# Optimization experiments

Hardware: AMD Instinct MI355X
Metric: run time of the kernel (lower is better)

The kernel has to match this reference:

```python
import jax, jax.numpy as jnp
import numpy as np

B, D, H, W, C = 8, 4, 56, 56, 128
HEADS = 4
WD, WH, WW = 2, 7, 7
SD, SH, SW = 1, 3, 3
N = WD * WH * WW            # tokens per window = 98
NW = (D // WD) * (H // WH) * (W // WW)  # windows per sample = 128
SCALE = (C // HEADS) ** -0.5
EPS = 1e-5


def _rel_pos_index():
    coords = np.stack(np.meshgrid(np.arange(WD), np.arange(WH), np.arange(WW), indexing='ij'))
    coords = coords.reshape(3, -1)                    # (3, N)
    rel = (coords[:, :, None] - coords[:, None, :]).transpose(1, 2, 0)  # (N, N, 3)
    rel[:, :, 0] += WD - 1
    rel[:, :, 1] += WH - 1
    rel[:, :, 2] += WW - 1
    rel[:, :, 0] *= (2 * WH - 1) * (2 * WW - 1)
    rel[:, :, 1] *= (2 * WW - 1)
    return rel.sum(-1)                                # (N, N) int

REL_IDX = jnp.asarray(_rel_pos_index())


def _np_window_partition(x, wd, wh, ww):
    b, d, h, w, c = x.shape
    x = x.reshape(b, d // wd, wd, h // wh, wh, w // ww, ww, c)
    return x.transpose(0, 1, 3, 5, 2, 4, 6, 7).reshape(-1, wd * wh * ww, c)


def _attn_mask():
    img = np.zeros((1, D, H, W, 1), np.float32)
    cnt = 0
    for ds in (slice(None, -WD), slice(-WD, -SD), slice(-SD, None)):
        for hs in (slice(None, -WH), slice(-WH, -SH), slice(-SH, None)):
            for ws in (slice(None, -WW), slice(-WW, -SW), slice(-SW, None)):
                img[:, ds, hs, ws, :] = cnt
                cnt += 1
    mw = _np_window_partition(img, WD, WH, WW)[..., 0]         # (nW, N)
    m = mw[:, None, :] - mw[:, :, None]                        # (nW, N, N)
    return jnp.asarray(np.where(m != 0, -100.0, 0.0).astype(np.float32))

ATTN_MASK = _attn_mask()  # (nW, N, N)


def window_partition(x):
    b = x.shape[0]
    x = x.reshape(b, D // WD, WD, H // WH, WH, W // WW, WW, C)
    return x.transpose(0, 1, 3, 5, 2, 4, 6, 7).reshape(-1, N, C)


def window_reverse(wins, b):
    x = wins.reshape(b, D // WD, H // WH, W // WW, WD, WH, WW, C)
    return x.transpose(0, 1, 4, 2, 5, 3, 6, 7).reshape(b, D, H, W, C)


def layernorm(x, g, b):
    mu = jnp.mean(x, axis=-1, keepdims=True)
    var = jnp.mean(jnp.square(x - mu), axis=-1, keepdims=True)
    return (x - mu) / jnp.sqrt(var + EPS) * g + b


def swin_block(x, norm1_g, norm1_b, qkv_w, qkv_b, rpb_table, proj_w, proj_b,
               norm2_g, norm2_b, fc1_w, fc1_b, fc2_w, fc2_b):
    shortcut = x
    h1 = layernorm(x, norm1_g, norm1_b)
    # cyclic shift (pad amounts are 0 for these dims)
    shifted = jnp.roll(h1, (-SD, -SH, -SW), axis=(1, 2, 3))
    xw = window_partition(shifted)                    # (B*nW, N, C)
    Bn = xw.shape[0]
    qkv = (xw @ qkv_w + qkv_b).reshape(Bn, N, 3, HEADS, C // HEADS)
    qkv = qkv.transpose(2, 0, 3, 1, 4)                # (3, Bn, h, N, c)
    q, k, v = qkv[0], qkv[1], qkv[2]
    attn = jnp.einsum('bhnc,bhmc->bhnm', q * SCALE, k)
    bias = rpb_table[REL_IDX].transpose(2, 0, 1)      # (h, N, N)
    attn = attn + bias[None]
    attn = attn.reshape(B, NW, HEADS, N, N) + ATTN_MASK[None, :, None]
    attn = jax.nn.softmax(attn.reshape(Bn, HEADS, N, N), axis=-1)
    out = jnp.einsum('bhnm,bhmc->bhnc', attn, v)
    out = out.transpose(0, 2, 1, 3).reshape(Bn, N, C)
    out = out @ proj_w + proj_b
    xr = window_reverse(out, B)
    xr = jnp.roll(xr, (SD, SH, SW), axis=(1, 2, 3))
    x1 = shortcut + xr
    h2 = layernorm(x1, norm2_g, norm2_b)
    mlp = jax.nn.gelu(h2 @ fc1_w + fc1_b, approximate=False) @ fc2_w + fc2_b
    return x1 + mlp


def setup_inputs() -> dict:
    key = jax.random.key(0)
    ks = jax.random.split(key, 6)
    s = 0.02
    return {
        'x': jax.random.normal(ks[0], (B, D, H, W, C), jnp.float32),
        'norm1_g': jnp.ones((C,), jnp.float32),
        'norm1_b': jnp.zeros((C,), jnp.float32),
        'qkv_w': jax.random.normal(ks[1], (C, 3 * C), jnp.float32) * s,
        'qkv_b': jnp.zeros((3 * C,), jnp.float32),
        'rpb_table': jax.random.normal(ks[2], ((2 * WD - 1) * (2 * WH - 1) * (2 * WW - 1), HEADS), jnp.float32) * s,
        'proj_w': jax.random.normal(ks[3], (C, C), jnp.float32) * s,
        'proj_b': jnp.zeros((C,), jnp.float32),
        'norm2_g': jnp.ones((C,), jnp.float32),
        'norm2_b': jnp.zeros((C,), jnp.float32),
        'fc1_w': jax.random.normal(ks[4], (C, 4 * C), jnp.float32) * s,
        'fc1_b': jnp.zeros((4 * C,), jnp.float32),
        'fc2_w': jax.random.normal(ks[5], (4 * C, C), jnp.float32) * s,
        'fc2_b': jnp.zeros((C,), jnp.float32),
    }


def reference(x, norm1_g, norm1_b, qkv_w, qkv_b, rpb_table, proj_w, proj_b,
              norm2_g, norm2_b, fc1_w, fc1_b, fc2_w, fc2_b):
    return swin_block(x, norm1_g, norm1_b, qkv_w, qkv_b, rpb_table, proj_w, proj_b,
                      norm2_g, norm2_b, fc1_w, fc1_b, fc2_w, fc2_b)
```

## Files before the change

### kernel.cpp

```cpp
#include <hip/hip_runtime.h>
#include <hip/hip_bf16.h>
#include <cstdint>
#include <cstddef>

using bf16 = __hip_bfloat16;
typedef __bf16 bf16x8 __attribute__((ext_vector_type(8)));
typedef float f32x4 __attribute__((ext_vector_type(4)));

#define DEV static __device__ __forceinline__

DEV bf16 f2b(float x) { return __float2bfloat16(x); }
DEV f32x4 mfma16(bf16x8 a, bf16x8 b, f32x4 c) {
    return __builtin_amdgcn_mfma_f32_16x16x32_bf16(a, b, c, 0, 0, 0);
}
DEV float gelu_f(float x) {
    float u2 = x * x;
    float u = x * (0.7978845608028654f + 0.0356774081363001f * u2);
    float s = 1.f / (1.f + __expf(-2.f * u));
    return x * s;
}
DEV void gload16(const bf16* g, bf16* l) {
    __builtin_amdgcn_global_load_lds(
        (const __attribute__((address_space(1))) unsigned int*)g,
        (__attribute__((address_space(3))) unsigned int*)l, 16, 0, 0);
}
DEV void stage16k(const bf16* __restrict__ g, bf16* l, int tid) {
    int w = tid >> 6, lane = tid & 63;
    #pragma unroll
    for (int j = 0; j < 4; ++j) {
        int blk = j * 4 + w;
        gload16(g + blk * 512 + lane * 8, l + blk * 512);
    }
}

constexpr int NTOK = 98;
constexpr int BNWIN = 1024;
constexpr int MTOT = BNWIN * NTOK;
constexpr float SCALE = 0.17677669529663687f;
constexpr float EPS = 1e-5f;

__global__ __launch_bounds__(256) void k_prep(const float* __restrict__ qkv_w,
        const float* __restrict__ proj_w, const float* __restrict__ fc1_w,
        const float* __restrict__ fc2_w, const float* __restrict__ rpb,
        bf16* __restrict__ QW, bf16* __restrict__ PW,
        bf16* __restrict__ W1, bf16* __restrict__ W2, float* __restrict__ BT) {
    int tid = blockIdx.x * 256 + threadIdx.x;
    int stride = gridDim.x * 256;
    for (int i = tid; i < 384 * 128; i += stride) {
        int n = i >> 7, k = i & 127;
        QW[i] = f2b(qkv_w[k * 384 + n]);
    }
    for (int i = tid; i < 128 * 128; i += stride) {
        int n = i >> 7, k = i & 127;
        PW[i] = f2b(proj_w[k * 128 + n]);
    }
    for (int i = tid; i < 512 * 128; i += stride) {
        int t = i >> 13, r = (i >> 7) & 63, kswz = i & 127;
        int k = kswz ^ ((r & 7) << 3);
        W1[i] = f2b(fc1_w[(size_t)k * 512 + t * 64 + r]);
    }
    for (int i = tid; i < 512 * 128; i += stride) {
        int t = i >> 13, c = (i >> 6) & 127, kswz = i & 63;
        int kk = kswz ^ ((c & 7) << 3);
        W2[i] = f2b(fc2_w[(size_t)(t * 64 + kk) * 128 + c]);
    }
    for (int i = tid; i < 4 * 98 * 98; i += stride) {
        int h = i / 9604, r = i - h * 9604;
        int ii = r / 98, jj = r - ii * 98;
        int di = ii >= 49, ri = ii - di * 49, hi = ri / 7, wi = ri - hi * 7;
        int dj = jj >= 49, rj = jj - dj * 49, hj = rj / 7, wj = rj - hj * 7;
        int bidx = (di - dj + 1) * 169 + (hi - hj + 6) * 13 + (wi - wj + 6);
        BT[i] = rpb[bidx * 4 + h];
    }
}

__global__ __launch_bounds__(256) void k_ln1(const float* __restrict__ x,
        const float* __restrict__ g, const float* __restrict__ be,
        bf16* __restrict__ xw) {
    int wave = threadIdx.x >> 6, lane = threadIdx.x & 63;
    int r = blockIdx.x * 4 + wave;
    int bn = r / 98, n = r - bn * 98;
    int b = bn >> 7, wr = bn & 127;
    int dB = wr >> 6, hB = (wr >> 3) & 7, wB = wr & 7;
    int dd = (n >= 49), rem = n - dd * 49;
    int hh = rem / 7, ww = rem - hh * 7;
    int dp = dB * 2 + dd, hp = hB * 7 + hh, wp = wB * 7 + ww;
    int ds = (dp + 1) & 3;
    int hs = hp + 3; if (hs >= 56) hs -= 56;
    int wsv = wp + 3; if (wsv >= 56) wsv -= 56;
    size_t src = ((size_t)((b * 4 + ds) * 56 + hs) * 56 + wsv) * 128;

    float2 v = *(const float2*)&x[src + lane * 2];
    float v0 = v.x, v1 = v.y;
    float s = v0 + v1, sq = v0 * v0 + v1 * v1;
    #pragma unroll
    for (int m = 1; m < 64; m <<= 1) { s += __shfl_xor(s, m); sq += __shfl_xor(sq, m); }
    float mean = s * (1.f / 128.f);
    float var = sq * (1.f / 128.f) - mean * mean;
    float rstd = rsqrtf(var + EPS);
    float g0 = g[lane * 2], g1 = g[lane * 2 + 1];
    float e0 = be[lane * 2], e1 = be[lane * 2 + 1];
    union { uint32_t u32; bf16 h[2]; } o;
    o.h[0] = f2b((v0 - mean) * rstd * g0 + e0);
    o.h[1] = f2b((v1 - mean) * rstd * g1 + e1);
    *(uint32_t*)&xw[(size_t)r * 128 + lane * 2] = o.u32;
}

__global__ __launch_bounds__(256) void k_qkv(const bf16* __restrict__ A,
        const bf16* __restrict__ QW, const float* __restrict__ bias,
        bf16* __restrict__ out) {
    __shared__ __align__(16) bf16 As[64 * 136];
    __shared__ __align__(16) bf16 Bt[64 * 136];
    int tid = threadIdx.x;
    int row0 = blockIdx.x * 64;
    int col0 = blockIdx.y * 64;
    #pragma unroll
    for (int p = 0; p < 4; ++p) {
        int vi = tid + p * 256;
        int row = vi >> 4, cg = vi & 15;
        *(uint4*)&As[row * 136 + cg * 8] =
            *(const uint4*)&A[(size_t)(row0 + row) * 128 + cg * 8];
    }
    #pragma unroll
    for (int p = 0; p < 4; ++p) {
        int vi = tid + p * 256;
        int row = vi >> 4, cg = vi & 15;
        *(uint4*)&Bt[row * 136 + cg * 8] =
            *(const uint4*)&QW[(size_t)(col0 + row) * 128 + cg * 8];
    }
    __syncthreads();
    int wave = tid >> 6, lane = tid & 63;
    int wr = (wave >> 1) * 32, wc = (wave & 1) * 32;
    int lrow = lane & 15, kg8 = (lane >> 4) * 8, g4 = (lane >> 4) * 4;
    f32x4 acc[2][2] = {};
    #pragma unroll
    for (int ksi = 0; ksi < 4; ++ksi) {
        bf16x8 a[2], bb[2];
        #pragma unroll
        for (int t = 0; t < 2; ++t)
            a[t] = *(const bf16x8*)&As[(wr + t * 16 + lrow) * 136 + ksi * 32 + kg8];
        #pragma unroll
        for (int u2 = 0; u2 < 2; ++u2)
            bb[u2] = *(const bf16x8*)&Bt[(wc + u2 * 16 + lrow) * 136 + ksi * 32 + kg8];
        #pragma unroll
        for (int t = 0; t < 2; ++t)
            #pragma unroll
            for (int u2 = 0; u2 < 2; ++u2)
                acc[t][u2] = mfma16(a[t], bb[u2], acc[t][u2]);
    }
    #pragma unroll
    for (int t = 0; t < 2; ++t)
        #pragma unroll
        for (int u2 = 0; u2 < 2; ++u2) {
            int gcol = col0 + wc + u2 * 16 + lrow;
            float bv = bias[gcol];
            #pragma unroll
            for (int r2 = 0; r2 < 4; ++r2) {
                int grow = row0 + wr + t * 16 + g4 + r2;
                out[(size_t)grow * 384 + gcol] = f2b(acc[t][u2][r2] + bv);
            }
        }
}

__global__ __launch_bounds__(256) void k_attn(const bf16* __restrict__ qkv,
        const float* __restrict__ BT, bf16* __restrict__ aout) {
    __shared__ __align__(16) bf16 qs[112 * 40];
    __shared__ __align__(16) bf16 ksm[112 * 40];
    __shared__ __align__(16) bf16 vt[32 * 136];
    __shared__ __align__(16) bf16 ps[112 * 136];
    __shared__ signed char trg[112];

    int tid = threadIdx.x;
    int bn = blockIdx.x, h = blockIdx.y;
    int wrw = bn & 127;
    int dB = wrw >> 6, hB = (wrw >> 3) & 7, wB = wrw & 7;

    {
        uint32_t* z1 = (uint32_t*)qs;
        uint32_t* z2 = (uint32_t*)ksm;
        for (int i = tid; i < 2240; i += 256) { z1[i] = 0u; z2[i] = 0u; }
        uint32_t* z3 = (uint32_t*)vt;
        for (int i = tid; i < 2176; i += 256) z3[i] = 0u;
        uint32_t* z4 = (uint32_t*)ps;
        for (int i = tid; i < 7616; i += 256) z4[i] = 0u;
    }
    if (tid < 112) {
        int n = tid < 98 ? tid : 97;
        int dd = n >= 49, rem = n - dd * 49;
        int hh = rem / 7, ww2 = rem - hh * 7;
        int dp = dB * 2 + dd, hp = hB * 7 + hh, wp = wB * 7 + ww2;
        int rd = dp < 2 ? 0 : (dp == 2 ? 1 : 2);
        int rh = hp < 49 ? 0 : (hp < 53 ? 1 : 2);
        int rw = wp < 49 ? 0 : (wp < 53 ? 1 : 2);
        trg[tid] = (signed char)(rd * 9 + rh * 3 + rw);
    }
    __syncthreads();
    const size_t base = (size_t)bn * 98 * 384 + h * 32;
    for (int ch = tid; ch < 1176; ch += 256) {
        int mat = ch / 392;
        int rem = ch - mat * 392;
        int row = rem >> 2, cg = rem & 3;
        uint4 v = *(const uint4*)&qkv[base + (size_t)row * 384 + mat * 128 + cg * 8];
        if (mat == 0)      *(uint4*)&qs[row * 40 + cg * 8] = v;
        else if (mat == 1) *(uint4*)&ksm[row * 40 + cg * 8] = v;
        else {
            const bf16* pv = (const bf16*)&v;
            #pragma unroll
            for (int j = 0; j < 8; ++j) vt[(cg * 8 + j) * 136 + row] = pv[j];
        }
    }
    __syncthreads();

    int wave = tid >> 6, lane = tid & 63;
    int lrow = lane & 15, kg8 = (lane >> 4) * 8, g4 = (lane >> 4) * 4;

    for (int rt = wave; rt < 7; rt += 4) {
        f32x4 sacc[7];
        bf16x8 qa = *(const bf16x8*)&qs[(rt * 16 + lrow) * 40 + kg8];
        #pragma unroll
        for (int ct = 0; ct < 7; ++ct) {
            bf16x8 kb = *(const bf16x8*)&ksm[(ct * 16 + lrow) * 40 + kg8];
            f32x4 z = {};
            sacc[ct] = mfma16(qa, kb, z);
        }
        #pragma unroll
        for (int r2 = 0; r2 < 4; ++r2) {
            int grow = rt * 16 + g4 + r2;
            int mi = grow < 98 ? grow : 97;
            int mrg = trg[mi];
            const float* btrow = &BT[((size_t)h * 98 + mi) * 98];
            float val[7];
            float mx = -1e30f;
            #pragma unroll
            for (int ct = 0; ct < 7; ++ct) {
                int jc = ct * 16 + lrow;
                int jj = jc < 98 ? jc : 97;
                float bias = btrow[jj];
                float mv = (mrg != (int)trg[jj]) ? -100.f : 0.f;
                float v = sacc[ct][r2] * SCALE + bias + mv;
                if (jc >= 98) v = -1e30f;
                val[ct] = v;
                mx = fmaxf(mx, v);
            }
            #pragma unroll
            for (int m = 1; m < 16; m <<= 1) mx = fmaxf(mx, __shfl_xor(mx, m));
            float sum = 0.f;
            #pragma unroll
            for (int ct = 0; ct < 7; ++ct) { val[ct] = __expf(val[ct] - mx); sum += val[ct]; }
            #pragma unroll
            for (int m = 1; m < 16; m <<= 1) sum += __shfl_xor(sum, m);
            float inv = 1.f / sum;
            #pragma unroll
            for (int ct = 0; ct < 7; ++ct)
                ps[grow * 136 + ct * 16 + lrow] = f2b(val[ct] * inv);
        }
        #pragma unroll
        for (int ct = 0; ct < 2; ++ct) {
            f32x4 oacc = {};
            #pragma unroll
            for (int ksi = 0; ksi < 4; ++ksi) {
                bf16x8 pa = *(const bf16x8*)&ps[(rt * 16 + lrow) * 136 + ksi * 32 + kg8];
                bf16x8 vb = *(const bf16x8*)&vt[(ct * 16 + lrow) * 136 + ksi * 32 + kg8];
                oacc = mfma16(pa, vb, oacc);
            }
            #pragma unroll
            for (int r2 = 0; r2 < 4; ++r2) {
                int grow = rt * 16 + g4 + r2;
                if (grow < 98)
                    aout[((size_t)bn * 98 + grow) * 128 + h * 32 + ct * 16 + lrow] =
                        f2b(oacc[r2]);
            }
        }
    }
}

__global__ __launch_bounds__(256) void k_proj(const bf16* __restrict__ A,
        const bf16* __restrict__ PW, const float* __restrict__ pb,
        const float* __restrict__ x, const float* __restrict__ g2,
        const float* __restrict__ be2,
        float* __restrict__ x1, bf16* __restrict__ h2) {
    __shared__ __align__(16) bf16 As[64 * 136];
    __shared__ __align__(16) bf16 Bt[128 * 136];
    int tid = threadIdx.x;
    int row0 = blockIdx.x * 64;
    #pragma unroll
    for (int p = 0; p < 4; ++p) {
        int vi = tid + p * 256;
        int row = vi >> 4, cg = vi & 15;
        *(uint4*)&As[row * 136 + cg * 8] =
            *(const uint4*)&A[(size_t)(row0 + row) * 128 + cg * 8];
    }
    #pragma unroll
    for (int p = 0; p < 8; ++p) {
        int vi = tid + p * 256;
        int row = vi >> 4, cg = vi & 15;
        *(uint4*)&Bt[row * 136 + cg * 8] =
            *(const uint4*)&PW[(size_t)row * 128 + cg * 8];
    }
    __syncthreads();
    int wave = tid >> 6, lane = tid & 63;
    int lrow = lane & 15, kg8 = (lane >> 4) * 8, g4 = (lane >> 4) * 4;
    f32x4 acc[8] = {};
    #pragma unroll
    for (int ksi = 0; ksi < 4; ++ksi) {
        bf16x8 a = *(const bf16x8*)&As[(wave * 16 + lrow) * 136 + ksi * 32 + kg8];
        #pragma unroll
        for (int ct = 0; ct < 8; ++ct) {
            bf16x8 bb = *(const bf16x8*)&Bt[(ct * 16 + lrow) * 136 + ksi * 32 + kg8];
            acc[ct] = mfma16(a, bb, acc[ct]);
        }
    }
    #pragma unroll
    for (int r2 = 0; r2 < 4; ++r2) {
        int rwin = row0 + wave * 16 + g4 + r2;
        int bn = rwin / 98, n = rwin - bn * 98;
        int b = bn >> 7, wr2 = bn & 127;
        int dB = wr2 >> 6, hB = (wr2 >> 3) & 7, wB = wr2 & 7;
        int dd = n >= 49, rem = n - dd * 49;
        int hh = rem / 7, ww2 = rem - hh * 7;
        int dp = dB * 2 + dd, hp = hB * 7 + hh, wp = wB * 7 + ww2;
        int d2 = (dp + 1) & 3;
        int hv = hp + 3; if (hv >= 56) hv -= 56;
        int wv = wp + 3; if (wv >= 56) wv -= 56;
        size_t dst = ((size_t)(b * 4 + d2) * 56 + hv) * 56 + wv;
        float vals[8], s = 0.f, sq = 0.f;
        #pragma unroll
        for (int ct = 0; ct < 8; ++ct) {
            int col = ct * 16 + lrow;
            float v = acc[ct][r2] + pb[col] + x[dst * 128 + col];
            vals[ct] = v; s += v; sq += v * v;
        }
        #pragma unroll
        for (int m = 1; m < 16; m <<= 1) { s += __shfl_xor(s, m); sq += __shfl_xor(sq, m); }
        float mean = s * (1.f / 128.f);
        float var = sq * (1.f / 128.f) - mean * mean;
        float rstd = rsqrtf(var + EPS);
        #pragma unroll
        for (int ct = 0; ct < 8; ++ct) {
            int col = ct * 16 + lrow;
            x1[dst * 128 + col] = vals[ct];
            h2[dst * 128 + col] = f2b((vals[ct] - mean) * rstd * g2[col] + be2[col]);
        }
    }
}

__global__ __launch_bounds__(256, 2) void k_mlp(const bf16* __restrict__ h2,
        const bf16* __restrict__ W1s, const float* __restrict__ b1,
        const bf16* __restrict__ W2s, const float* __restrict__ b2v,
        const float* __restrict__ x1, float* __restrict__ out) {
    __shared__ __align__(16) bf16 W1b[2][8192];
    __shared__ __align__(16) bf16 W2b[2][8192];
    __shared__ __align__(16) bf16 Ts[64 * 72];
    int tid = threadIdx.x;
    int row0 = blockIdx.x * 64;
    int wave = tid >> 6, lane = tid & 63;
    int lrow = lane & 15, kg8 = (lane >> 4) * 8, g4 = (lane >> 4) * 4;
    int swz = (lrow & 7) << 3;

    stage16k(W1s, W1b[0], tid);
    stage16k(W2s, W2b[0], tid);

    bf16x8 a1[4];
    const bf16* arow = &h2[(size_t)(row0 + wave * 16 + lrow) * 128];
    #pragma unroll
    for (int ksi = 0; ksi < 4; ++ksi)
        a1[ksi] = *(const bf16x8*)&arow[ksi * 32 + kg8];

    __syncthreads();

    f32x4 oacc[8] = {};
    int n = 0;
    for (int hc = 0; hc < 8; ++hc) {
        if (hc < 7) {
            stage16k(W1s + (hc + 1) * 8192, W1b[n ^ 1], tid);
            stage16k(W2s + (hc + 1) * 8192, W2b[n ^ 1], tid);
        }
        f32x4 tacc[4] = {};
        #pragma unroll
        for (int ksi = 0; ksi < 4; ++ksi) {
            int k0 = ksi * 32 + kg8;
            #pragma unroll
            for (int ct = 0; ct < 4; ++ct) {
                bf16x8 bb = *(const bf16x8*)&W1b[n][(ct * 16 + lrow) * 128 + (k0 ^ swz)];
                tacc[ct] = mfma16(a1[ksi], bb, tacc[ct]);
            }
        }
        #pragma unroll
        for (int ct = 0; ct < 4; ++ct) {
            int hcol = hc * 64 + ct * 16 + lrow;
            float bb = b1[hcol];
            #pragma unroll
            for (int r2 = 0; r2 < 4; ++r2) {
                float t = gelu_f(tacc[ct][r2] + bb);
                Ts[(wave * 16 + g4 + r2) * 72 + ct * 16 + lrow] = f2b(t);
            }
        }
        #pragma unroll
        for (int ksi = 0; ksi < 2; ++ksi) {
            int k0 = ksi * 32 + kg8;
            bf16x8 a = *(const bf16x8*)&Ts[(wave * 16 + lrow) * 72 + k0];
            #pragma unroll
            for (int ct = 0; ct < 8; ++ct) {
                bf16x8 bb = *(const bf16x8*)&W2b[n][(ct * 16 + lrow) * 64 + (k0 ^ swz)];
                oacc[ct] = mfma16(a, bb, oacc[ct]);
            }
        }
        __syncthreads();
        n ^= 1;
    }
    #pragma unroll
    for (int ct = 0; ct < 8; ++ct) {
        int col = ct * 16 + lrow;
        float bb = b2v[col];
        #pragma unroll
        for (int r2 = 0; r2 < 4; ++r2) {
            size_t grow = (size_t)row0 + wave * 16 + g4 + r2;
            out[grow * 128 + col] = oacc[ct][r2] + bb + x1[grow * 128 + col];
        }
    }
}

extern "C" void kernel_launch(void* const* d_in, const int* in_sizes, int n_in,
                              void* d_out, int out_size, void* d_ws, size_t ws_size,
                              hipStream_t stream) {
    (void)in_sizes; (void)n_in; (void)out_size; (void)ws_size;
    const float* x      = (const float*)d_in[0];
    const float* n1g    = (const float*)d_in[1];
    const float* n1b    = (const float*)d_in[2];
    const float* qkv_w  = (const float*)d_in[3];
    const float* qkv_b  = (const float*)d_in[4];
    const float* rpb    = (const float*)d_in[5];
    const float* proj_w = (const float*)d_in[6];
    const float* proj_b = (const float*)d_in[7];
    const float* n2g    = (const float*)d_in[8];
    const float* n2b    = (const float*)d_in[9];
    const float* fc1_w  = (const float*)d_in[10];
    const float* fc1_b  = (const float*)d_in[11];
    const float* fc2_w  = (const float*)d_in[12];
    const float* fc2_b  = (const float*)d_in[13];
    float* outp = (float*)d_out;

    char* ws = (char*)d_ws;
    constexpr size_t S = (size_t)MTOT * 128 * 2;
    bf16*  xw     = (bf16*)ws;
    bf16*  qkvbuf = (bf16*)(ws + S);
    bf16*  aout   = xw;
    float* x1     = (float*)(ws + S);
    bf16*  h2     = (bf16*)(ws + 3 * S);
    char* wp_ = ws + 4 * S;
    bf16*  QW  = (bf16*)wp_;
    bf16*  PW  = (bf16*)(wp_ + 98304);
    bf16*  W1s = (bf16*)(wp_ + 98304 + 32768);
    bf16*  W2s = (bf16*)(wp_ + 98304 + 32768 + 131072);
    float* BTb = (float*)(wp_ + 98304 + 32768 + 131072 + 131072);

    k_prep<<<192, 256, 0, stream>>>(qkv_w, proj_w, fc1_w, fc2_w, rpb, QW, PW, W1s, W2s, BTb);
    k_ln1 <<<MTOT / 4, 256, 0, stream>>>(x, n1g, n1b, xw);
    k_qkv <<<dim3(MTOT / 64, 6), 256, 0, stream>>>(xw, QW, qkv_b, qkvbuf);
    k_attn<<<dim3(BNWIN, 4), 256, 0, stream>>>(qkvbuf, BTb, aout);
    k_proj<<<MTOT / 64, 256, 0, stream>>>(aout, PW, proj_b, x, n2g, n2b, x1, h2);
    k_mlp <<<MTOT / 64, 256, 0, stream>>>(h2, W1s, fc1_b, W2s, fc2_b, x1, outp);
}
```

Before: 234.3 us.

## Enlarge MLP tiles to 128 rows, single-buffer weights, shrink attention P buffer

The MLP kernel now runs 512-thread blocks covering 128 rows. Each staged weight chunk is shared by twice as many rows, and double buffering is replaced by a single buffer loaded at the start of each hidden chunk. This halves the weight traffic per row and cuts LDS use, but the loads are no longer overlapped with compute, so each chunk waits on a synchronous load. The attention kernel's probability scratch shrinks to a per-wave 64-row buffer, which lowers shared memory and the zeroing work and may raise occupancy.

```diff
diff --git a/kernel.cpp b/kernel.cpp
--- a/kernel.cpp
+++ b/kernel.cpp
@@ -23,14 +23,6 @@
     __builtin_amdgcn_global_load_lds(
         (const __attribute__((address_space(1))) unsigned int*)g,
         (__attribute__((address_space(3))) unsigned int*)l, 16, 0, 0);
-}
-DEV void stage16k(const bf16* __restrict__ g, bf16* l, int tid) {
-    int w = tid >> 6, lane = tid & 63;
-    #pragma unroll
-    for (int j = 0; j < 4; ++j) {
-        int blk = j * 4 + w;
-        gload16(g + blk * 512 + lane * 8, l + blk * 512);
-    }
 }
 
 constexpr int NTOK = 98;
@@ -167,7 +159,7 @@
     __shared__ __align__(16) bf16 qs[112 * 40];
     __shared__ __align__(16) bf16 ksm[112 * 40];
     __shared__ __align__(16) bf16 vt[32 * 136];
-    __shared__ __align__(16) bf16 ps[112 * 136];
+    __shared__ __align__(16) bf16 ps[64 * 136];
     __shared__ signed char trg[112];
 
     int tid = threadIdx.x;
@@ -182,7 +174,7 @@
         uint32_t* z3 = (uint32_t*)vt;
         for (int i = tid; i < 2176; i += 256) z3[i] = 0u;
         uint32_t* z4 = (uint32_t*)ps;
-        for (int i = tid; i < 7616; i += 256) z4[i] = 0u;
+        for (int i = tid; i < 4352; i += 256) z4[i] = 0u;
     }
     if (tid < 112) {
         int n = tid < 98 ? tid : 97;
@@ -252,14 +244,14 @@
             float inv = 1.f / sum;
             #pragma unroll
             for (int ct = 0; ct < 7; ++ct)
-                ps[grow * 136 + ct * 16 + lrow] = f2b(val[ct] * inv);
+                ps[(wave * 16 + g4 + r2) * 136 + ct * 16 + lrow] = f2b(val[ct] * inv);
         }
         #pragma unroll
         for (int ct = 0; ct < 2; ++ct) {
             f32x4 oacc = {};
             #pragma unroll
             for (int ksi = 0; ksi < 4; ++ksi) {
-                bf16x8 pa = *(const bf16x8*)&ps[(rt * 16 + lrow) * 136 + ksi * 32 + kg8];
+                bf16x8 pa = *(const bf16x8*)&ps[(wave * 16 + lrow) * 136 + ksi * 32 + kg8];
                 bf16x8 vb = *(const bf16x8*)&vt[(ct * 16 + lrow) * 136 + ksi * 32 + kg8];
                 oacc = mfma16(pa, vb, oacc);
             }
@@ -344,44 +336,44 @@
     }
 }
 
-__global__ __launch_bounds__(256, 2) void k_mlp(const bf16* __restrict__ h2,
+__global__ __launch_bounds__(512) void k_mlp(const bf16* __restrict__ h2,
         const bf16* __restrict__ W1s, const float* __restrict__ b1,
         const bf16* __restrict__ W2s, const float* __restrict__ b2v,
         const float* __restrict__ x1, float* __restrict__ out) {
-    __shared__ __align__(16) bf16 W1b[2][8192];
-    __shared__ __align__(16) bf16 W2b[2][8192];
-    __shared__ __align__(16) bf16 Ts[64 * 72];
+    __shared__ __align__(16) bf16 W1b[8192];
+    __shared__ __align__(16) bf16 W2b[8192];
+    __shared__ __align__(16) bf16 Ts[128 * 72];
     int tid = threadIdx.x;
-    int row0 = blockIdx.x * 64;
+    int row0 = blockIdx.x * 128;
     int wave = tid >> 6, lane = tid & 63;
     int lrow = lane & 15, kg8 = (lane >> 4) * 8, g4 = (lane >> 4) * 4;
     int swz = (lrow & 7) << 3;
 
-    stage16k(W1s, W1b[0], tid);
-    stage16k(W2s, W2b[0], tid);
-
     bf16x8 a1[4];
     const bf16* arow = &h2[(size_t)(row0 + wave * 16 + lrow) * 128];
     #pragma unroll
     for (int ksi = 0; ksi < 4; ++ksi)
         a1[ksi] = *(const bf16x8*)&arow[ksi * 32 + kg8];
 
-    __syncthreads();
-
     f32x4 oacc[8] = {};
-    int n = 0;
     for (int hc = 0; hc < 8; ++hc) {
-        if (hc < 7) {
-            stage16k(W1s + (hc + 1) * 8192, W1b[n ^ 1], tid);
-            stage16k(W2s + (hc + 1) * 8192, W2b[n ^ 1], tid);
-        }
+        const bf16* W1g = W1s + hc * 8192;
+        const bf16* W2g = W2s + hc * 8192;
+        #pragma unroll
+        for (int j = 0; j < 4; ++j) {
+            int chunk = wave + j * 8;
+            if (chunk < 16) gload16(W1g + chunk * 512 + lane * 8, W1b + chunk * 512);
+            else            gload16(W2g + (chunk - 16) * 512 + lane * 8, W2b + (chunk - 16) * 512);
+        }
+        __syncthreads();
+
         f32x4 tacc[4] = {};
         #pragma unroll
         for (int ksi = 0; ksi < 4; ++ksi) {
             int k0 = ksi * 32 + kg8;
             #pragma unroll
             for (int ct = 0; ct < 4; ++ct) {
-                bf16x8 bb = *(const bf16x8*)&W1b[n][(ct * 16 + lrow) * 128 + (k0 ^ swz)];
+                bf16x8 bb = *(const bf16x8*)&W1b[(ct * 16 + lrow) * 128 + (k0 ^ swz)];
                 tacc[ct] = mfma16(a1[ksi], bb, tacc[ct]);
             }
         }
@@ -401,12 +393,11 @@
             bf16x8 a = *(const bf16x8*)&Ts[(wave * 16 + lrow) * 72 + k0];
             #pragma unroll
             for (int ct = 0; ct < 8; ++ct) {
-                bf16x8 bb = *(const bf16x8*)&W2b[n][(ct * 16 + lrow) * 64 + (k0 ^ swz)];
+                bf16x8 bb = *(const bf16x8*)&W2b[(ct * 16 + lrow) * 64 + (k0 ^ swz)];
                 oacc[ct] = mfma16(a, bb, oacc[ct]);
             }
         }
         __syncthreads();
-        n ^= 1;
     }
     #pragma unroll
     for (int ct = 0; ct < 8; ++ct) {
@@ -459,5 +450,5 @@
     k_qkv <<<dim3(MTOT / 64, 6), 256, 0, stream>>>(xw, QW, qkv_b, qkvbuf);
     k_attn<<<dim3(BNWIN, 4), 256, 0, stream>>>(qkvbuf, BTb, aout);
     k_proj<<<MTOT / 64, 256, 0, stream>>>(aout, PW, proj_b, x, n2g, n2b, x1, h2);
-    k_mlp <<<MTOT / 64, 256, 0, stream>>>(h2, W1s, fc1_b, W2s, fc2_b, x1, outp);
-}
+    k_mlp <<<MTOT / 128, 512, 0, stream>>>(h2, W1s, fc1_b, W2s, fc2_b, x1, outp);
+}
```

Result: faster. 221.7 us (-5.4%).
